# Performance work log

Hardware: AMD Instinct MI355X
Metric: run time of the kernel (lower is better)

The kernel has to match this reference:

```python
import jax, jax.numpy as jnp
import numpy as np

B, L, D, S = 8, 512, 64, 8


def setup_inputs() -> dict:
    key = jax.random.key(0)
    ks = jax.random.split(key, 8)
    return {
        "lstm1": jax.random.normal(ks[0], (B, L, D), dtype=jnp.float32),
        "lstm2": jax.random.normal(ks[1], (B, L, D), dtype=jnp.float32),
        "W": jax.random.normal(ks[2], (S, D, D), dtype=jnp.float32) * 0.1,
        "V": jax.random.normal(ks[3], (S, 2 * D), dtype=jnp.float32) * 0.1,
        "b": jax.random.normal(ks[4], (S,), dtype=jnp.float32) * 0.1,
        "W_g": jax.random.normal(ks[5], (S, 2 * D), dtype=jnp.float32) * 0.1,
        "b_g": jax.random.normal(ks[6], (S,), dtype=jnp.float32) * 0.1,
        "u": jax.random.normal(ks[7], (1, S), dtype=jnp.float32) * 0.1,
    }


def reference(lstm1, lstm2, W, V, b, W_g, b_g, u):
    # lstm1/lstm2: (B, L, D). Pairwise slot (i, j) pairs lstm1[:, i] with lstm2[:, j].
    d = lstm1.shape[-1]
    # Bilinear tensor-network score: x1_i W_s x2_j -> (B, L, L, S)
    result_w = jnp.einsum('bid,sde,bje->bijs', lstm1, W, lstm2)
    # concat(x1_i, x2_j) @ V^T decomposed to avoid materializing (B,L,L,2D)
    v1 = jnp.einsum('bid,sd->bis', lstm1, V[:, :d])[:, :, None, :]   # (B,L,1,S)
    v2 = jnp.einsum('bjd,sd->bjs', lstm2, V[:, d:])[:, None, :, :]   # (B,1,L,S)
    result_v = v1 + v2                                               # (B,L,L,S)
    g1 = jnp.einsum('bid,sd->bis', lstm1, W_g[:, :d])[:, :, None, :]
    g2 = jnp.einsum('bjd,sd->bjs', lstm2, W_g[:, d:])[:, None, :, :]
    gate = jax.nn.sigmoid(g1 + g2 + b_g)                             # (B,L,L,S)
    result_final = gate * result_w + (1.0 - gate) * jax.nn.sigmoid(result_v) + b
    # Reduce slices with u (shape (1,S)) -> (B,L,L), then add singleton channel dim.
    out = jnp.einsum('bijs,ks->bijk', result_final, u)[..., 0]
    return out[:, None, :, :]  # (B, 1, L, L)
```

## Files before the change

kernel.cpp:

```cpp
#include <hip/hip_runtime.h>
#include <math.h>

typedef float f32x4 __attribute__((ext_vector_type(4)));
typedef short bf16x8 __attribute__((ext_vector_type(8)));

namespace {
constexpr int kB = 8, kL = 512, kD = 64, kS = 8;
constexpr size_t SCL_OFF = 0;
constexpr size_t T_OFF   = 524288;
}

__device__ __forceinline__ unsigned short f2bf(float f) {
    unsigned u = __float_as_uint(f);
    u += 0x7FFFu + ((u >> 16) & 1u);
    return (unsigned short)(u >> 16);
}
__device__ __forceinline__ unsigned pk2(float lo, float hi) {
    return (unsigned)f2bf(lo) | ((unsigned)f2bf(hi) << 16);
}
__device__ __forceinline__ bf16x8 ldcvt8(const float* __restrict__ p) {
    const float4 a = *(const float4*)p;
    const float4 b = *(const float4*)(p + 4);
    union { bf16x8 v; uint4 q; } cv;
    cv.q.x = pk2(a.x, a.y); cv.q.y = pk2(a.z, a.w);
    cv.q.z = pk2(b.x, b.y); cv.q.w = pk2(b.z, b.w);
    return cv.v;
}

__global__ __launch_bounds__(256) void grn_a(
    const float* __restrict__ lstm1, const float* __restrict__ lstm2,
    const float* __restrict__ W, const float* __restrict__ V,
    const float* __restrict__ Wg, const float* __restrict__ bg,
    unsigned char* __restrict__ ws)
{
    __shared__ float wsm[64][68];
    __shared__ __align__(16) unsigned short tls[4][16][72];
    float* scl = (float*)(ws + SCL_OFF);
    unsigned short* T = (unsigned short*)(ws + T_OFF);
    const int tid = threadIdx.x;
    if (blockIdx.x < 64) {
        const int rb = blockIdx.x;
        const int b = rb >> 3, r0 = (rb & 7) * 64;
        const int kind = tid & 3, row = r0 + (tid >> 2);
        const float* x = (kind < 2 ? lstm1 : lstm2) + ((size_t)b * kL + row) * kD;
        float xr[64];
        #pragma unroll
        for (int q = 0; q < 16; q++)
            *(float4*)&xr[q * 4] = *(const float4*)(x + q * 4);
        const float* vb = ((kind & 1) ? Wg : V) + ((kind & 2) ? kD : 0);
        #pragma unroll
        for (int s = 0; s < kS; s++) {
            const float* vec = vb + s * 2 * kD;
            float a = 0.f;
            #pragma unroll
            for (int q = 0; q < 16; q++) {
                const float4 vv = *(const float4*)(vec + q * 4);
                a = fmaf(vv.x, xr[q * 4 + 0], a);
                a = fmaf(vv.y, xr[q * 4 + 1], a);
                a = fmaf(vv.z, xr[q * 4 + 2], a);
                a = fmaf(vv.w, xr[q * 4 + 3], a);
            }
            const float badd = (kind == 1) ? bg[s] : 0.f;
            scl[(((size_t)kind * 8 + b) * 8 + s) * 512 + row] = __expf(-(a + badd));
        }
        return;
    }
    const int t = blockIdx.x - 64;
    const int b = t >> 6, rem = t & 63, s = rem >> 3, i64 = rem & 7;
    {
        const float* pw = W + s * 4096;
        const int row = tid >> 2, c0 = (tid & 3) * 16;
        #pragma unroll
        for (int q = 0; q < 4; q++)
            *(float4*)&wsm[row][c0 + q * 4] = *(const float4*)(pw + row * 64 + c0 + q * 4);
    }
    __syncthreads();
    const int lane = tid & 63, w = tid >> 6;
    const int fr = lane & 15, fh = lane >> 4;
    const int i0 = i64 * 64 + w * 16;
    const float* ap = lstm1 + (((size_t)b * kL + i0 + fr) * kD + fh * 8);
    const bf16x8 A0 = ldcvt8(ap);
    const bf16x8 A1 = ldcvt8(ap + 32);
    unsigned short (*__restrict__ tw)[72] = tls[w];
    #pragma unroll
    for (int ne = 0; ne < 4; ne++) {
        union { bf16x8 v; uint4 q; } B0, B1;
        const int e = ne * 16 + fr;
        B0.q.x = pk2(wsm[fh * 8 + 0][e], wsm[fh * 8 + 1][e]);
        B0.q.y = pk2(wsm[fh * 8 + 2][e], wsm[fh * 8 + 3][e]);
        B0.q.z = pk2(wsm[fh * 8 + 4][e], wsm[fh * 8 + 5][e]);
        B0.q.w = pk2(wsm[fh * 8 + 6][e], wsm[fh * 8 + 7][e]);
        B1.q.x = pk2(wsm[32 + fh * 8 + 0][e], wsm[32 + fh * 8 + 1][e]);
        B1.q.y = pk2(wsm[32 + fh * 8 + 2][e], wsm[32 + fh * 8 + 3][e]);
        B1.q.z = pk2(wsm[32 + fh * 8 + 4][e], wsm[32 + fh * 8 + 5][e]);
        B1.q.w = pk2(wsm[32 + fh * 8 + 6][e], wsm[32 + fh * 8 + 7][e]);
        f32x4 z = {0.f, 0.f, 0.f, 0.f};
        f32x4 d = __builtin_amdgcn_mfma_f32_16x16x32_bf16(A0, B0.v, z, 0, 0, 0);
        d = __builtin_amdgcn_mfma_f32_16x16x32_bf16(A1, B1.v, d, 0, 0, 0);
        #pragma unroll
        for (int r = 0; r < 4; r++)
            tw[fh * 4 + r][ne * 16 + fr] = f2bf(d[r]);
    }
    const int rr = lane >> 2, cc = (lane & 3) * 16;
    const uint4 q0 = *(const uint4*)&tw[rr][cc];
    const uint4 q1 = *(const uint4*)&tw[rr][cc + 8];
    unsigned short* tp = T + (((size_t)(b * 8 + s)) * kL + i0 + rr) * kD + cc;
    *(uint4*)tp = q0;
    *(uint4*)(tp + 8) = q1;
}

__global__ __launch_bounds__(256) void grn_b(
    const float* __restrict__ lstm2, const float* __restrict__ bS,
    const float* __restrict__ u, const unsigned char* __restrict__ ws,
    float* __restrict__ out)
{
    const float* scl = (const float*)(ws + SCL_OFF);
    const unsigned short* T = (const unsigned short*)(ws + T_OFF);
    const int g = blockIdx.x * 4 + (threadIdx.x >> 6);
    const int b = g >> 9, rem = g & 511, it = rem >> 4, j32 = rem & 15;
    const int lane = threadIdx.x & 63, fr = lane & 15, fh = lane >> 4;
    const int i0 = it * 16, j0 = j32 * 32;
    bf16x8 Bf[2][2];
    #pragma unroll
    for (int jj = 0; jj < 2; jj++) {
        const float* bp = lstm2 + (((size_t)b * kL + j0 + jj * 16 + fr) * kD + fh * 8);
        Bf[jj][0] = ldcvt8(bp);
        Bf[jj][1] = ldcvt8(bp + 32);
    }
    float bias_c = 0.f;
    #pragma unroll
    for (int s = 0; s < kS; s++) bias_c = fmaf(u[s], bS[s], bias_c);
    f32x4 oacc[2];
    oacc[0] = f32x4{bias_c, bias_c, bias_c, bias_c};
    oacc[1] = oacc[0];
    #pragma unroll
    for (int s = 0; s < kS; s++) {
        const unsigned short* ap = T + (((size_t)(b * 8 + s)) * kL + i0 + fr) * kD + fh * 8;
        const bf16x8 A0 = *(const bf16x8*)ap;
        const bf16x8 A1 = *(const bf16x8*)(ap + 32);
        const float4 E1vq = *(const float4*)(scl + (((size_t)0 * 8 + b) * 8 + s) * 512 + i0 + fh * 4);
        const float4 E1gq = *(const float4*)(scl + (((size_t)1 * 8 + b) * 8 + s) * 512 + i0 + fh * 4);
        const float us = u[s];
        const float E1va[4] = {E1vq.x, E1vq.y, E1vq.z, E1vq.w};
        const float E1ga[4] = {E1gq.x, E1gq.y, E1gq.z, E1gq.w};
        #pragma unroll
        for (int jj = 0; jj < 2; jj++) {
            f32x4 z = {0.f, 0.f, 0.f, 0.f};
            f32x4 acc = __builtin_amdgcn_mfma_f32_16x16x32_bf16(A0, Bf[jj][0], z, 0, 0, 0);
            acc = __builtin_amdgcn_mfma_f32_16x16x32_bf16(A1, Bf[jj][1], acc, 0, 0, 0);
            const int j = j0 + jj * 16 + fr;
            const float E2v = scl[(((size_t)2 * 8 + b) * 8 + s) * 512 + j];
            const float E2g = scl[(((size_t)3 * 8 + b) * 8 + s) * 512 + j];
            #pragma unroll
            for (int r = 0; r < 4; r++) {
                const float dg = fmaf(E1ga[r], E2g, 1.f);
                const float dv = fmaf(E1va[r], E2v, 1.f);
                const float rp = __builtin_amdgcn_rcpf(dg * dv);
                const float gate = dv * rp;
                const float sv   = dg * rp;
                const float res = fmaf(gate, acc[r] - sv, sv);
                oacc[jj][r] = fmaf(us, res, oacc[jj][r]);
            }
        }
    }
    #pragma unroll
    for (int jj = 0; jj < 2; jj++) {
        float* op = out + (((size_t)b * kL + i0 + fh * 4) * kL + j0 + jj * 16 + fr);
        #pragma unroll
        for (int r = 0; r < 4; r++)
            op[(size_t)r * kL] = oacc[jj][r];
    }
}

extern "C" void kernel_launch(void* const* d_in, const int* in_sizes, int n_in,
                              void* d_out, int out_size, void* d_ws, size_t ws_size,
                              hipStream_t stream) {
    const float* lstm1 = (const float*)d_in[0];
    const float* lstm2 = (const float*)d_in[1];
    const float* W     = (const float*)d_in[2];
    const float* V     = (const float*)d_in[3];
    const float* bS    = (const float*)d_in[4];
    const float* Wg    = (const float*)d_in[5];
    const float* bg    = (const float*)d_in[6];
    const float* u     = (const float*)d_in[7];
    unsigned char* ws = (unsigned char*)d_ws;
    grn_a<<<576, 256, 0, stream>>>(lstm1, lstm2, W, V, Wg, bg, ws);
    grn_b<<<1024, 256, 0, stream>>>(lstm2, bS, u, ws, (float*)d_out);
}
```

Measured before the change: 105.2 us.

## Precompute W·x2 instead of x1·W and swizzle block order in grn_b

Changes the bilinear factorization so the first kernel computes U = W_s·lstm2_j (stored per j) rather than T = lstm1_i·W_s. The W matrix is now loaded straight from global memory into MFMA fragments, which removes the shared-memory staging buffer and its barrier. The second kernel then uses lstm1 rows as the resident A operand and streams U per slot, with a block-index swizzle that spreads consecutive blocks across batches. Mapping outputs to 32x16 tiles changes the store pattern and the scale-vector access, which could affect coalescing.

```diff
diff --git a/kernel.cpp b/kernel.cpp
--- a/kernel.cpp
+++ b/kernel.cpp
@@ -7,7 +7,7 @@
 namespace {
 constexpr int kB = 8, kL = 512, kD = 64, kS = 8;
 constexpr size_t SCL_OFF = 0;
-constexpr size_t T_OFF   = 524288;
+constexpr size_t U_OFF   = 524288;
 }
 
 __device__ __forceinline__ unsigned short f2bf(float f) {
@@ -33,10 +33,9 @@
     const float* __restrict__ Wg, const float* __restrict__ bg,
     unsigned char* __restrict__ ws)
 {
-    __shared__ float wsm[64][68];
     __shared__ __align__(16) unsigned short tls[4][16][72];
     float* scl = (float*)(ws + SCL_OFF);
-    unsigned short* T = (unsigned short*)(ws + T_OFF);
+    unsigned short* Ut = (unsigned short*)(ws + U_OFF);
     const int tid = threadIdx.x;
     if (blockIdx.x < 64) {
         const int rb = blockIdx.x;
@@ -66,66 +65,52 @@
         return;
     }
     const int t = blockIdx.x - 64;
-    const int b = t >> 6, rem = t & 63, s = rem >> 3, i64 = rem & 7;
-    {
-        const float* pw = W + s * 4096;
-        const int row = tid >> 2, c0 = (tid & 3) * 16;
-        #pragma unroll
-        for (int q = 0; q < 4; q++)
-            *(float4*)&wsm[row][c0 + q * 4] = *(const float4*)(pw + row * 64 + c0 + q * 4);
-    }
-    __syncthreads();
+    const int b = t >> 6, rem = t & 63, s = rem >> 3, j64 = rem & 7;
     const int lane = tid & 63, w = tid >> 6;
     const int fr = lane & 15, fh = lane >> 4;
-    const int i0 = i64 * 64 + w * 16;
-    const float* ap = lstm1 + (((size_t)b * kL + i0 + fr) * kD + fh * 8);
-    const bf16x8 A0 = ldcvt8(ap);
-    const bf16x8 A1 = ldcvt8(ap + 32);
+    const int j0 = j64 * 64 + w * 16;
+    const float* bp = lstm2 + (((size_t)b * kL + j0 + fr) * kD + fh * 8);
+    const bf16x8 B0 = ldcvt8(bp);
+    const bf16x8 B1 = ldcvt8(bp + 32);
     unsigned short (*__restrict__ tw)[72] = tls[w];
     #pragma unroll
-    for (int ne = 0; ne < 4; ne++) {
-        union { bf16x8 v; uint4 q; } B0, B1;
-        const int e = ne * 16 + fr;
-        B0.q.x = pk2(wsm[fh * 8 + 0][e], wsm[fh * 8 + 1][e]);
-        B0.q.y = pk2(wsm[fh * 8 + 2][e], wsm[fh * 8 + 3][e]);
-        B0.q.z = pk2(wsm[fh * 8 + 4][e], wsm[fh * 8 + 5][e]);
-        B0.q.w = pk2(wsm[fh * 8 + 6][e], wsm[fh * 8 + 7][e]);
-        B1.q.x = pk2(wsm[32 + fh * 8 + 0][e], wsm[32 + fh * 8 + 1][e]);
-        B1.q.y = pk2(wsm[32 + fh * 8 + 2][e], wsm[32 + fh * 8 + 3][e]);
-        B1.q.z = pk2(wsm[32 + fh * 8 + 4][e], wsm[32 + fh * 8 + 5][e]);
-        B1.q.w = pk2(wsm[32 + fh * 8 + 6][e], wsm[32 + fh * 8 + 7][e]);
+    for (int dt = 0; dt < 4; dt++) {
+        const float* ap = W + ((size_t)s * 4096 + (dt * 16 + fr) * kD + fh * 8);
+        const bf16x8 A0 = ldcvt8(ap);
+        const bf16x8 A1 = ldcvt8(ap + 32);
         f32x4 z = {0.f, 0.f, 0.f, 0.f};
-        f32x4 d = __builtin_amdgcn_mfma_f32_16x16x32_bf16(A0, B0.v, z, 0, 0, 0);
-        d = __builtin_amdgcn_mfma_f32_16x16x32_bf16(A1, B1.v, d, 0, 0, 0);
+        f32x4 d = __builtin_amdgcn_mfma_f32_16x16x32_bf16(A0, B0, z, 0, 0, 0);
+        d = __builtin_amdgcn_mfma_f32_16x16x32_bf16(A1, B1, d, 0, 0, 0);
         #pragma unroll
         for (int r = 0; r < 4; r++)
-            tw[fh * 4 + r][ne * 16 + fr] = f2bf(d[r]);
+            tw[fr][dt * 16 + fh * 4 + r] = f2bf(d[r]);
     }
     const int rr = lane >> 2, cc = (lane & 3) * 16;
     const uint4 q0 = *(const uint4*)&tw[rr][cc];
     const uint4 q1 = *(const uint4*)&tw[rr][cc + 8];
-    unsigned short* tp = T + (((size_t)(b * 8 + s)) * kL + i0 + rr) * kD + cc;
-    *(uint4*)tp = q0;
-    *(uint4*)(tp + 8) = q1;
+    unsigned short* up = Ut + (((size_t)(b * 8 + s)) * kL + j0 + rr) * kD + cc;
+    *(uint4*)up = q0;
+    *(uint4*)(up + 8) = q1;
 }
 
 __global__ __launch_bounds__(256) void grn_b(
-    const float* __restrict__ lstm2, const float* __restrict__ bS,
+    const float* __restrict__ lstm1, const float* __restrict__ bS,
     const float* __restrict__ u, const unsigned char* __restrict__ ws,
     float* __restrict__ out)
 {
     const float* scl = (const float*)(ws + SCL_OFF);
-    const unsigned short* T = (const unsigned short*)(ws + T_OFF);
-    const int g = blockIdx.x * 4 + (threadIdx.x >> 6);
-    const int b = g >> 9, rem = g & 511, it = rem >> 4, j32 = rem & 15;
+    const unsigned short* Ut = (const unsigned short*)(ws + U_OFF);
+    const int swz = (blockIdx.x & 7) * 128 + (blockIdx.x >> 3);
+    const int g = swz * 4 + (threadIdx.x >> 6);
+    const int b = g >> 9, rem = g & 511, i32 = rem >> 5, jt = rem & 31;
     const int lane = threadIdx.x & 63, fr = lane & 15, fh = lane >> 4;
-    const int i0 = it * 16, j0 = j32 * 32;
-    bf16x8 Bf[2][2];
+    const int i0 = i32 * 32, j0 = jt * 16;
+    bf16x8 A[2][2];
     #pragma unroll
-    for (int jj = 0; jj < 2; jj++) {
-        const float* bp = lstm2 + (((size_t)b * kL + j0 + jj * 16 + fr) * kD + fh * 8);
-        Bf[jj][0] = ldcvt8(bp);
-        Bf[jj][1] = ldcvt8(bp + 32);
+    for (int ii = 0; ii < 2; ii++) {
+        const float* ap = lstm1 + (((size_t)b * kL + i0 + ii * 16 + fr) * kD + fh * 8);
+        A[ii][0] = ldcvt8(ap);
+        A[ii][1] = ldcvt8(ap + 32);
     }
     float bias_c = 0.f;
     #pragma unroll
@@ -135,22 +120,22 @@
     oacc[1] = oacc[0];
     #pragma unroll
     for (int s = 0; s < kS; s++) {
-        const unsigned short* ap = T + (((size_t)(b * 8 + s)) * kL + i0 + fr) * kD + fh * 8;
-        const bf16x8 A0 = *(const bf16x8*)ap;
-        const bf16x8 A1 = *(const bf16x8*)(ap + 32);
-        const float4 E1vq = *(const float4*)(scl + (((size_t)0 * 8 + b) * 8 + s) * 512 + i0 + fh * 4);
-        const float4 E1gq = *(const float4*)(scl + (((size_t)1 * 8 + b) * 8 + s) * 512 + i0 + fh * 4);
+        const unsigned short* bp = Ut + (((size_t)(b * 8 + s)) * kL + j0 + fr) * kD + fh * 8;
+        const bf16x8 B0 = *(const bf16x8*)bp;
+        const bf16x8 B1 = *(const bf16x8*)(bp + 32);
+        const float E2v = scl[(((size_t)2 * 8 + b) * 8 + s) * 512 + j0 + fr];
+        const float E2g = scl[(((size_t)3 * 8 + b) * 8 + s) * 512 + j0 + fr];
         const float us = u[s];
-        const float E1va[4] = {E1vq.x, E1vq.y, E1vq.z, E1vq.w};
-        const float E1ga[4] = {E1gq.x, E1gq.y, E1gq.z, E1gq.w};
         #pragma unroll
-        for (int jj = 0; jj < 2; jj++) {
+        for (int ii = 0; ii < 2; ii++) {
             f32x4 z = {0.f, 0.f, 0.f, 0.f};
-            f32x4 acc = __builtin_amdgcn_mfma_f32_16x16x32_bf16(A0, Bf[jj][0], z, 0, 0, 0);
-            acc = __builtin_amdgcn_mfma_f32_16x16x32_bf16(A1, Bf[jj][1], acc, 0, 0, 0);
-            const int j = j0 + jj * 16 + fr;
-            const float E2v = scl[(((size_t)2 * 8 + b) * 8 + s) * 512 + j];
-            const float E2g = scl[(((size_t)3 * 8 + b) * 8 + s) * 512 + j];
+            f32x4 acc = __builtin_amdgcn_mfma_f32_16x16x32_bf16(A[ii][0], B0, z, 0, 0, 0);
+            acc = __builtin_amdgcn_mfma_f32_16x16x32_bf16(A[ii][1], B1, acc, 0, 0, 0);
+            const int ib = i0 + ii * 16 + fh * 4;
+            const float4 E1vq = *(const float4*)(scl + (((size_t)0 * 8 + b) * 8 + s) * 512 + ib);
+            const float4 E1gq = *(const float4*)(scl + (((size_t)1 * 8 + b) * 8 + s) * 512 + ib);
+            const float E1va[4] = {E1vq.x, E1vq.y, E1vq.z, E1vq.w};
+            const float E1ga[4] = {E1gq.x, E1gq.y, E1gq.z, E1gq.w};
             #pragma unroll
             for (int r = 0; r < 4; r++) {
                 const float dg = fmaf(E1ga[r], E2g, 1.f);
@@ -159,16 +144,16 @@
                 const float gate = dv * rp;
                 const float sv   = dg * rp;
                 const float res = fmaf(gate, acc[r] - sv, sv);
-                oacc[jj][r] = fmaf(us, res, oacc[jj][r]);
+                oacc[ii][r] = fmaf(us, res, oacc[ii][r]);
             }
         }
     }
     #pragma unroll
-    for (int jj = 0; jj < 2; jj++) {
-        float* op = out + (((size_t)b * kL + i0 + fh * 4) * kL + j0 + jj * 16 + fr);
+    for (int ii = 0; ii < 2; ii++) {
+        float* op = out + (((size_t)b * kL + i0 + ii * 16 + fh * 4) * kL + j0 + fr);
         #pragma unroll
         for (int r = 0; r < 4; r++)
-            op[(size_t)r * kL] = oacc[jj][r];
+            op[(size_t)r * kL] = oacc[ii][r];
     }
 }
 
@@ -185,5 +170,5 @@
     const float* u     = (const float*)d_in[7];
     unsigned char* ws = (unsigned char*)d_ws;
     grn_a<<<576, 256, 0, stream>>>(lstm1, lstm2, W, V, Wg, bg, ws);
-    grn_b<<<1024, 256, 0, stream>>>(lstm2, bS, u, ws, (float*)d_out);
+    grn_b<<<1024, 256, 0, stream>>>(lstm1, bS, u, ws, (float*)d_out);
 }
```

Result: no change. 106.3 us (+1.1%).
